# Performance work log

Measured on AMD Instinct MI355X. Metric: run time of the kernel, lower is better.

The kernel has to match this reference:

```python
import jax, jax.numpy as jnp
import numpy as np
import math


def _mixed_masks(seq_len, local_scope, num_heads, dtype=jnp.float32):
    # 4 mask groups: global (none), local band, forward (j>=i), backward (j<=i)
    i = jnp.arange(seq_len)[:, None]
    j = jnp.arange(seq_len)[None, :]
    ninf = jnp.array(-jnp.inf, dtype)
    zero = jnp.zeros((seq_len, seq_len), dtype)
    g = zero
    l = jnp.where(jnp.abs(i - j) <= local_scope, 0.0, ninf).astype(dtype)
    f = jnp.where(i > j, ninf, 0.0).astype(dtype)  # keep j >= i
    b = jnp.where(i < j, ninf, 0.0).astype(dtype)  # keep j <= i
    masks = jnp.stack([g, l, f, b], axis=0)  # [4, T, T]
    # tf.repeat(..., num_heads//4, axis=0): g,g,...,l,l,...,f,...,b,...
    return jnp.repeat(masks, num_heads // 4, axis=0)  # [H, T, T]


def setup_inputs() -> dict:
    key = jax.random.key(0)
    ks = jax.random.split(key, 6)
    B, T, D, H, dk = 2, 2048, 512, 8, 64
    return {
        "query": jax.random.normal(ks[0], (B, T, D), jnp.float32),
        "value": jax.random.normal(ks[1], (B, T, D), jnp.float32),
        "Wq": jax.random.normal(ks[2], (H, D, dk), jnp.float32) * 0.02,
        "Wk": jax.random.normal(ks[3], (H, D, dk), jnp.float32) * 0.02,
        "Wv": jax.random.normal(ks[4], (H, D, dk), jnp.float32) * 0.02,
        "Wo": jax.random.normal(ks[5], (H, dk, D), jnp.float32) * 0.02,
        "local_scope": 4,
    }


def reference(query, value, Wq, Wk, Wv, Wo, local_scope):
    B, T, D = query.shape
    H, _, dk = Wq.shape
    masks = _mixed_masks(T, local_scope, H, query.dtype)  # [H, T, T]
    # projections: 'abx,cxd->acbd'
    q = jnp.einsum('btd,hdk->bhtk', query, Wq)
    k = jnp.einsum('bsd,hdk->bhsk', value, Wk)  # key defaults to value
    v = jnp.einsum('bsd,hdk->bhsk', value, Wv)
    scores = jnp.einsum('bhtk,bhsk->bhts', q, k) / math.sqrt(dk)
    scores = scores + masks[None]  # broadcast over batch
    # Keras Softmax(axis=[-1,-2]): joint softmax over both last axes
    probs = jax.nn.softmax(scores, axis=(-2, -1))
    att = jnp.einsum('bhts,bhsk->bhtk', probs, v)
    # output projection: 'axby,xyc->abc'
    out = jnp.einsum('bhtk,hkd->btd', att, Wo)
    return out
```

## Files before the change

kernel.cpp:

```cpp
#include <hip/hip_runtime.h>
#include <math.h>

#define T_SEQ  2048
#define D_MODEL 512
#define NH     8
#define DK     64
#define NKB    32
#define BH     16
#define HK     512
#define NCH    2
#define CHB    16
#define LOG2E  1.44269504088896340736f
#define QSCALE (0.125f * LOG2E)

typedef unsigned int uint;
typedef unsigned short ushort;
typedef __attribute__((ext_vector_type(8))) short bf16x8;
typedef __attribute__((ext_vector_type(4))) float f32x4;

#define QHI_B   (0ull)
#define QLO_B   (QHI_B + 4194304ull)
#define KHI_B   (QLO_B + 4194304ull)
#define KLO_B   (KHI_B + 4194304ull)
#define VTHI_B  (KLO_B + 4194304ull)
#define VTLO_B  (VTHI_B + 4194304ull)
#define WTHI_B  (VTLO_B + 4194304ull)
#define WTLO_B  (WTHI_B + 1572864ull)
#define WOTHI_B (WTLO_B + 1572864ull)
#define WOTLO_B (WOTHI_B + 524288ull)
#define ATTP_B  (WOTLO_B + 524288ull)
#define CHUNK_F 2097152ull
#define MST_B   (ATTP_B + (ull_t)NCH * 8388608ull)
#define LST_B   (MST_B + 262144ull)
#define SST_B   (LST_B + 262144ull)
#define ATTSHI_B (SST_B + 262144ull)
#define ATTSLO_B (ATTSHI_B + 4194304ull)
typedef unsigned long long ull_t;

static __device__ __forceinline__ void tsplit2(float a, float b, uint& hi, uint& lo) {
    uint ua = __float_as_uint(a), ub = __float_as_uint(b);
    uint ha = ua & 0xFFFF0000u, hb = ub & 0xFFFF0000u;
    hi = (ha >> 16) | hb;
    float ra = a - __uint_as_float(ha);
    float rb = b - __uint_as_float(hb);
    lo = (__float_as_uint(ra) >> 16) | (__float_as_uint(rb) & 0xFFFF0000u);
}

__global__ __launch_bounds__(256) void split_w(
    const float* __restrict__ Wq, const float* __restrict__ Wk,
    const float* __restrict__ Wv, const float* __restrict__ Wo,
    float* __restrict__ ws)
{
    uint* WTH = (uint*)((char*)ws + WTHI_B);
    uint* WTL = (uint*)((char*)ws + WTLO_B);
    uint* WOH = (uint*)((char*)ws + WOTHI_B);
    uint* WOL = (uint*)((char*)ws + WOTLO_B);
    const int gid = blockIdx.x * 256 + threadIdx.x;
    if (blockIdx.x < 1536) {
        const int d2 = gid & 255;
        const int k = (gid >> 8) & 63;
        const int h = (gid >> 14) & 7;
        const int which = gid >> 17;
        const float* W = (which == 0 ? Wq : (which == 1 ? Wk : Wv));
        const float* src = W + ((size_t)h * D_MODEL + 2 * d2) * DK + k;
        uint hi, lo;
        tsplit2(src[0], src[DK], hi, lo);
        const size_t o = (((size_t)(which * 8 + h) * 64 + k) * 512 + 2 * d2) >> 1;
        WTH[o] = hi; WTL[o] = lo;
    } else {
        const int o = gid - 1536 * 256;
        const int hk2 = o & 255;
        const int d = o >> 8;
        const float* src = Wo + (size_t)(2 * hk2) * D_MODEL + d;
        uint hi, lo;
        tsplit2(src[0], src[D_MODEL], hi, lo);
        const size_t oo = ((size_t)d * 512 + 2 * hk2) >> 1;
        WOH[oo] = hi; WOL[oo] = lo;
    }
}

__global__ __launch_bounds__(256) void proj_mfma(
    const float* __restrict__ query, const float* __restrict__ value,
    float* __restrict__ ws)
{
    const int which = blockIdx.z;
    const int bh = blockIdx.y, b = bh >> 3, h = bh & 7;
    const int t0 = blockIdx.x * 64;
    const float* X = (which == 0 ? query : value) + (size_t)b * T_SEQ * D_MODEL;
    const ushort* WtH = (const ushort*)((char*)ws + WTHI_B) + (size_t)(which * 8 + h) * 64 * 512;
    const ushort* WtL = (const ushort*)((char*)ws + WTLO_B) + (size_t)(which * 8 + h) * 64 * 512;

    __shared__ ushort BsH[64][64], BsL[64][64];

    const int tid = threadIdx.x, lane = tid & 63, w = tid >> 6;
    const int lr = lane & 15, lg = lane >> 4;
    const int sg = tid & 7, srow = tid >> 3;
    const int swz0 = (sg ^ (srow & 7)) * 8;
    const int c0s = (lg ^ (lr & 7)) * 8, c1s = c0s ^ 32;

    f32x4 acc[4];
#pragma unroll
    for (int i = 0; i < 4; ++i) acc[i] = (f32x4){0.f, 0.f, 0.f, 0.f};

    for (int d0 = 0; d0 < D_MODEL; d0 += 64) {
        __syncthreads();
        *(uint4*)&BsH[srow][swz0]      = *(const uint4*)&WtH[(size_t)srow * 512 + d0 + sg * 8];
        *(uint4*)&BsH[srow + 32][swz0] = *(const uint4*)&WtH[(size_t)(srow + 32) * 512 + d0 + sg * 8];
        *(uint4*)&BsL[srow][swz0]      = *(const uint4*)&WtL[(size_t)srow * 512 + d0 + sg * 8];
        *(uint4*)&BsL[srow + 32][swz0] = *(const uint4*)&WtL[(size_t)(srow + 32) * 512 + d0 + sg * 8];
        __syncthreads();

        const float* xr = &X[(size_t)(t0 + w * 16 + lr) * D_MODEL + d0];
        float x0[8], x1[8];
        *(float4*)&x0[0] = *(const float4*)(xr + lg * 8);
        *(float4*)&x0[4] = *(const float4*)(xr + lg * 8 + 4);
        *(float4*)&x1[0] = *(const float4*)(xr + 32 + lg * 8);
        *(float4*)&x1[4] = *(const float4*)(xr + 32 + lg * 8 + 4);
        union { bf16x8 v; uint u[4]; } xh0, xl0, xh1, xl1;
#pragma unroll
        for (int i = 0; i < 4; ++i) {
            tsplit2(x0[2 * i], x0[2 * i + 1], xh0.u[i], xl0.u[i]);
            tsplit2(x1[2 * i], x1[2 * i + 1], xh1.u[i], xl1.u[i]);
        }

#pragma unroll
        for (int m2 = 0; m2 < 4; ++m2) {
            const int row = m2 * 16 + lr;
            bf16x8 wh0 = *(const bf16x8*)&BsH[row][c0s];
            bf16x8 wh1 = *(const bf16x8*)&BsH[row][c1s];
            bf16x8 wl0 = *(const bf16x8*)&BsL[row][c0s];
            bf16x8 wl1 = *(const bf16x8*)&BsL[row][c1s];
            f32x4 a = acc[m2];
            if (which < 2) {
                a = __builtin_amdgcn_mfma_f32_16x16x32_bf16(wh0, xh0.v, a, 0, 0, 0);
                a = __builtin_amdgcn_mfma_f32_16x16x32_bf16(wh1, xh1.v, a, 0, 0, 0);
                a = __builtin_amdgcn_mfma_f32_16x16x32_bf16(wh0, xl0.v, a, 0, 0, 0);
                a = __builtin_amdgcn_mfma_f32_16x16x32_bf16(wh1, xl1.v, a, 0, 0, 0);
                a = __builtin_amdgcn_mfma_f32_16x16x32_bf16(wl0, xh0.v, a, 0, 0, 0);
                a = __builtin_amdgcn_mfma_f32_16x16x32_bf16(wl1, xh1.v, a, 0, 0, 0);
            } else {
                a = __builtin_amdgcn_mfma_f32_16x16x32_bf16(xh0.v, wh0, a, 0, 0, 0);
                a = __builtin_amdgcn_mfma_f32_16x16x32_bf16(xh1.v, wh1, a, 0, 0, 0);
                a = __builtin_amdgcn_mfma_f32_16x16x32_bf16(xl0.v, wh0, a, 0, 0, 0);
                a = __builtin_amdgcn_mfma_f32_16x16x32_bf16(xl1.v, wh1, a, 0, 0, 0);
                a = __builtin_amdgcn_mfma_f32_16x16x32_bf16(xh0.v, wl0, a, 0, 0, 0);
                a = __builtin_amdgcn_mfma_f32_16x16x32_bf16(xh1.v, wl1, a, 0, 0, 0);
            }
            acc[m2] = a;
        }
    }

    if (which < 2) {
        ushort* OH = (ushort*)((char*)ws + (which == 0 ? QHI_B : KHI_B)) + (size_t)bh * T_SEQ * DK;
        ushort* OL = (ushort*)((char*)ws + (which == 0 ? QLO_B : KLO_B)) + (size_t)bh * T_SEQ * DK;
        const float scl = (which == 0) ? QSCALE : 1.0f;
#pragma unroll
        for (int m2 = 0; m2 < 4; ++m2) {
            uint h0, l0, h1, l1;
            tsplit2(acc[m2][0] * scl, acc[m2][1] * scl, h0, l0);
            tsplit2(acc[m2][2] * scl, acc[m2][3] * scl, h1, l1);
            const size_t addr = (size_t)(t0 + w * 16 + lr) * DK + m2 * 16 + lg * 4;
            *(uint2*)&OH[addr] = make_uint2(h0, h1);
            *(uint2*)&OL[addr] = make_uint2(l0, l1);
        }
    } else {
        ushort* OH = (ushort*)((char*)ws + VTHI_B) + (size_t)bh * DK * T_SEQ;
        ushort* OL = (ushort*)((char*)ws + VTLO_B) + (size_t)bh * DK * T_SEQ;
#pragma unroll
        for (int n2 = 0; n2 < 4; ++n2) {
            uint h0, l0, h1, l1;
            tsplit2(acc[n2][0], acc[n2][1], h0, l0);
            tsplit2(acc[n2][2], acc[n2][3], h1, l1);
            const size_t addr = (size_t)(n2 * 16 + lr) * T_SEQ + t0 + w * 16 + lg * 4;
            *(uint2*)&OH[addr] = make_uint2(h0, h1);
            *(uint2*)&OL[addr] = make_uint2(l0, l1);
        }
    }
}

__global__ __launch_bounds__(256, 3) void attn_fwd(
    const int* __restrict__ ls_ptr, float* __restrict__ ws)
{
    const int bh = blockIdx.y, b = bh >> 3, h = bh & 7;
    const int mtype = h >> 1;
    const int row0 = blockIdx.x * 64, rb = row0 >> 6;
    const int chunk = blockIdx.z;
    const int ls = *ls_ptr;

    float* mrow = (float*)((char*)ws + MST_B) + ((size_t)chunk * BH + bh) * T_SEQ;
    float* lrow = (float*)((char*)ws + LST_B) + ((size_t)chunk * BH + bh) * T_SEQ;

    int klo = 0, khi = NKB - 1;
    if (mtype == 1) {
        int l2 = row0 - ls; if (l2 < 0) l2 = 0;
        int h2 = row0 + 63 + ls; if (h2 > T_SEQ - 1) h2 = T_SEQ - 1;
        klo = l2 >> 6; khi = h2 >> 6;
    } else if (mtype == 2) {
        klo = rb;
    } else if (mtype == 3) {
        khi = rb;
    }
    const int kb0 = klo > chunk * CHB ? klo : chunk * CHB;
    const int kb1 = khi < chunk * CHB + CHB - 1 ? khi : chunk * CHB + CHB - 1;

    const int tid = threadIdx.x;
    if (kb0 > kb1) {
        if (tid < 64) { mrow[row0 + tid] = -INFINITY; lrow[row0 + tid] = 0.f; }
        return;
    }

    const ushort* Qh_g = (const ushort*)((char*)ws + QHI_B) + (size_t)bh * T_SEQ * DK;
    const ushort* Ql_g = (const ushort*)((char*)ws + QLO_B) + (size_t)bh * T_SEQ * DK;
    const ushort* Kh_g = (const ushort*)((char*)ws + KHI_B) + (size_t)bh * T_SEQ * DK;
    const ushort* Kl_g = (const ushort*)((char*)ws + KLO_B) + (size_t)bh * T_SEQ * DK;
    const ushort* Vh_g = (const ushort*)((char*)ws + VTHI_B) + (size_t)bh * DK * T_SEQ;
    const ushort* Vl_g = (const ushort*)((char*)ws + VTLO_B) + (size_t)bh * DK * T_SEQ;
    float* attP = (float*)((char*)ws + ATTP_B) + (size_t)chunk * CHUNK_F;

    __shared__ ushort KhS[64][64], KlS[64][64];
    __shared__ ushort VhS[64][64], VlS[64][64];
    __shared__ ushort PhS[64][64], PlS[64][64];

    const int lane = tid & 63, w = tid >> 6;
    const int lr = lane & 15, lg = lane >> 4;
    const int sg = tid & 7, srow = tid >> 3;
    const int swz0 = (sg ^ (srow & 7)) * 8;
    const int c0s = (lg ^ (lr & 7)) * 8, c1s = c0s ^ 32;

    const ushort* qh = Qh_g + (size_t)(row0 + w * 16 + lr) * DK;
    const ushort* ql = Ql_g + (size_t)(row0 + w * 16 + lr) * DK;
    const bf16x8 bqh0 = *(const bf16x8*)(qh + lg * 8);
    const bf16x8 bqh1 = *(const bf16x8*)(qh + 32 + lg * 8);
    const bf16x8 bql0 = *(const bf16x8*)(ql + lg * 8);
    const bf16x8 bql1 = *(const bf16x8*)(ql + 32 + lg * 8);

    float m_i = -INFINITY, l_i = 0.f;
    f32x4 oacc[4];
#pragma unroll
    for (int i = 0; i < 4; ++i) oacc[i] = (f32x4){0.f, 0.f, 0.f, 0.f};

    uint4 kr0, kr1, kr2, kr3, vr0, vr1, vr2, vr3;
    kr0 = *(const uint4*)&Kh_g[(size_t)(kb0 * 64 + srow) * DK + sg * 8];
    kr1 = *(const uint4*)&Kh_g[(size_t)(kb0 * 64 + srow + 32) * DK + sg * 8];
    kr2 = *(const uint4*)&Kl_g[(size_t)(kb0 * 64 + srow) * DK + sg * 8];
    kr3 = *(const uint4*)&Kl_g[(size_t)(kb0 * 64 + srow + 32) * DK + sg * 8];
    vr0 = *(const uint4*)&Vh_g[(size_t)srow * T_SEQ + kb0 * 64 + sg * 8];
    vr1 = *(const uint4*)&Vh_g[(size_t)(srow + 32) * T_SEQ + kb0 * 64 + sg * 8];
    vr2 = *(const uint4*)&Vl_g[(size_t)srow * T_SEQ + kb0 * 64 + sg * 8];
    vr3 = *(const uint4*)&Vl_g[(size_t)(srow + 32) * T_SEQ + kb0 * 64 + sg * 8];

    for (int kb = kb0; kb <= kb1; ++kb) {
        __syncthreads();
        *(uint4*)&KhS[srow][swz0] = kr0; *(uint4*)&KhS[srow + 32][swz0] = kr1;
        *(uint4*)&KlS[srow][swz0] = kr2; *(uint4*)&KlS[srow + 32][swz0] = kr3;
        *(uint4*)&VhS[srow][swz0] = vr0; *(uint4*)&VhS[srow + 32][swz0] = vr1;
        *(uint4*)&VlS[srow][swz0] = vr2; *(uint4*)&VlS[srow + 32][swz0] = vr3;
        if (kb < kb1) {
            const int kn = kb + 1;
            kr0 = *(const uint4*)&Kh_g[(size_t)(kn * 64 + srow) * DK + sg * 8];
            kr1 = *(const uint4*)&Kh_g[(size_t)(kn * 64 + srow + 32) * DK + sg * 8];
            kr2 = *(const uint4*)&Kl_g[(size_t)(kn * 64 + srow) * DK + sg * 8];
            kr3 = *(const uint4*)&Kl_g[(size_t)(kn * 64 + srow + 32) * DK + sg * 8];
            vr0 = *(const uint4*)&Vh_g[(size_t)srow * T_SEQ + kn * 64 + sg * 8];
            vr1 = *(const uint4*)&Vh_g[(size_t)(srow + 32) * T_SEQ + kn * 64 + sg * 8];
            vr2 = *(const uint4*)&Vl_g[(size_t)srow * T_SEQ + kn * 64 + sg * 8];
            vr3 = *(const uint4*)&Vl_g[(size_t)(srow + 32) * T_SEQ + kn * 64 + sg * 8];
        }
        __syncthreads();

        f32x4 sacc[4];
#pragma unroll
        for (int m = 0; m < 4; ++m) {
            const int row = m * 16 + lr;
            bf16x8 ah0 = *(const bf16x8*)&KhS[row][c0s];
            bf16x8 ah1 = *(const bf16x8*)&KhS[row][c1s];
            bf16x8 al0 = *(const bf16x8*)&KlS[row][c0s];
            bf16x8 al1 = *(const bf16x8*)&KlS[row][c1s];
            f32x4 a = (f32x4){0.f, 0.f, 0.f, 0.f};
            a = __builtin_amdgcn_mfma_f32_16x16x32_bf16(ah0, bqh0, a, 0, 0, 0);
            a = __builtin_amdgcn_mfma_f32_16x16x32_bf16(ah1, bqh1, a, 0, 0, 0);
            a = __builtin_amdgcn_mfma_f32_16x16x32_bf16(ah0, bql0, a, 0, 0, 0);
            a = __builtin_amdgcn_mfma_f32_16x16x32_bf16(ah1, bql1, a, 0, 0, 0);
            a = __builtin_amdgcn_mfma_f32_16x16x32_bf16(al0, bqh0, a, 0, 0, 0);
            a = __builtin_amdgcn_mfma_f32_16x16x32_bf16(al1, bqh1, a, 0, 0, 0);
            sacc[m] = a;
        }

        const int t_glob = row0 + w * 16 + lr;
        const bool needmask = (mtype == 1) || ((mtype >= 2) && (kb == rb));
        float p[4][4];
        float vmax = -INFINITY;
#pragma unroll
        for (int m = 0; m < 4; ++m)
#pragma unroll
            for (int r = 0; r < 4; ++r) {
                float x = sacc[m][r];
                if (needmask) {
                    int s_glob = kb * 64 + m * 16 + lg * 4 + r;
                    bool keep;
                    if (mtype == 1) keep = (t_glob - s_glob <= ls) && (s_glob - t_glob <= ls);
                    else if (mtype == 2) keep = (s_glob >= t_glob);
                    else keep = (s_glob <= t_glob);
                    if (!keep) x = -INFINITY;
                }
                p[m][r] = x;
                vmax = fmaxf(vmax, x);
            }
        vmax = fmaxf(vmax, __shfl_xor(vmax, 16, 64));
        vmax = fmaxf(vmax, __shfl_xor(vmax, 32, 64));
        const float mn = fmaxf(m_i, vmax);
        float factor = 1.f, psum = 0.f;
        if (mn == -INFINITY) {
#pragma unroll
            for (int m = 0; m < 4; ++m)
#pragma unroll
                for (int r = 0; r < 4; ++r) p[m][r] = 0.f;
        } else {
            factor = exp2f(m_i - mn);
            m_i = mn;
#pragma unroll
            for (int m = 0; m < 4; ++m)
#pragma unroll
                for (int r = 0; r < 4; ++r) {
                    p[m][r] = exp2f(p[m][r] - mn);
                    psum += p[m][r];
                }
        }
        psum += __shfl_xor(psum, 16, 64);
        psum += __shfl_xor(psum, 32, 64);
        l_i = l_i * factor + psum;

#pragma unroll
        for (int m = 0; m < 4; ++m) {
            uint ph01, pl01, ph23, pl23;
            tsplit2(p[m][0], p[m][1], ph01, pl01);
            tsplit2(p[m][2], p[m][3], ph23, pl23);
            const int pg = (((m * 2 + (lg >> 1)) ^ (lr & 7)) * 8) + (lg & 1) * 4;
            *(uint2*)&PhS[w * 16 + lr][pg] = make_uint2(ph01, ph23);
            *(uint2*)&PlS[w * 16 + lr][pg] = make_uint2(pl01, pl23);
        }

        float fr[4];
#pragma unroll
        for (int r = 0; r < 4; ++r) fr[r] = __shfl(factor, lg * 4 + r, 64);
#pragma unroll
        for (int n2 = 0; n2 < 4; ++n2)
#pragma unroll
            for (int r = 0; r < 4; ++r) oacc[n2][r] *= fr[r];

        const bf16x8 aph0 = *(const bf16x8*)&PhS[w * 16 + lr][c0s];
        const bf16x8 aph1 = *(const bf16x8*)&PhS[w * 16 + lr][c1s];
        const bf16x8 apl0 = *(const bf16x8*)&PlS[w * 16 + lr][c0s];
        const bf16x8 apl1 = *(const bf16x8*)&PlS[w * 16 + lr][c1s];
#pragma unroll
        for (int n2 = 0; n2 < 4; ++n2) {
            const int row = n2 * 16 + lr;
            bf16x8 bh0 = *(const bf16x8*)&VhS[row][c0s];
            bf16x8 bh1 = *(const bf16x8*)&VhS[row][c1s];
            bf16x8 bl0 = *(const bf16x8*)&VlS[row][c0s];
            bf16x8 bl1 = *(const bf16x8*)&VlS[row][c1s];
            f32x4 a = oacc[n2];
            a = __builtin_amdgcn_mfma_f32_16x16x32_bf16(aph0, bh0, a, 0, 0, 0);
            a = __builtin_amdgcn_mfma_f32_16x16x32_bf16(aph1, bh1, a, 0, 0, 0);
            a = __builtin_amdgcn_mfma_f32_16x16x32_bf16(aph0, bl0, a, 0, 0, 0);
            a = __builtin_amdgcn_mfma_f32_16x16x32_bf16(aph1, bl1, a, 0, 0, 0);
            a = __builtin_amdgcn_mfma_f32_16x16x32_bf16(apl0, bh0, a, 0, 0, 0);
            a = __builtin_amdgcn_mfma_f32_16x16x32_bf16(apl1, bh1, a, 0, 0, 0);
            oacc[n2] = a;
        }
    }

#pragma unroll
    for (int n2 = 0; n2 < 4; ++n2)
#pragma unroll
        for (int r = 0; r < 4; ++r) {
            int t = row0 + w * 16 + lg * 4 + r;
            attP[((size_t)b * T_SEQ + t) * HK + h * DK + n2 * 16 + lr] = oacc[n2][r];
        }
    if (lg == 0) {
        mrow[row0 + w * 16 + lr] = m_i;
        lrow[row0 + w * 16 + lr] = l_i;
    }
}

__global__ __launch_bounds__(256) void softmax_stats(float* __restrict__ ws)
{
    const int bh = blockIdx.x;
    float* mbase = (float*)((char*)ws + MST_B);
    float* lbase = (float*)((char*)ws + LST_B);
    float* sbase = (float*)((char*)ws + SST_B);

    __shared__ float red[256];
    const int tid = threadIdx.x;
    const int n = NCH * T_SEQ;

    float mymax = -INFINITY;
    for (int i = tid; i < n; i += 256) {
        int c = i >> 11, t = i & 2047;
        mymax = fmaxf(mymax, mbase[((size_t)c * BH + bh) * T_SEQ + t]);
    }
    red[tid] = mymax; __syncthreads();
    for (int s = 128; s > 0; s >>= 1) {
        if (tid < s) red[tid] = fmaxf(red[tid], red[tid + s]);
        __syncthreads();
    }
    const float M = red[0]; __syncthreads();

    float mysum = 0.f;
    for (int i = tid; i < n; i += 256) {
        int c = i >> 11, t = i & 2047;
        size_t idx = ((size_t)c * BH + bh) * T_SEQ + t;
        mysum += lbase[idx] * exp2f(mbase[idx] - M);
    }
    red[tid] = mysum; __syncthreads();
    for (int s = 128; s > 0; s >>= 1) {
        if (tid < s) red[tid] += red[tid + s];
        __syncthreads();
    }
    const float Z = red[0];

    for (int i = tid; i < n; i += 256) {
        int c = i >> 11, t = i & 2047;
        size_t idx = ((size_t)c * BH + bh) * T_SEQ + t;
        sbase[idx] = exp2f(mbase[idx] - M) / Z;
    }
}

__global__ __launch_bounds__(256) void reduce_split(float* __restrict__ ws)
{
    const size_t flat = ((size_t)blockIdx.x * 256 + threadIdx.x) * 4;
    const float* attP = (const float*)((char*)ws + ATTP_B);
    const float* sc = (const float*)((char*)ws + SST_B);
    ushort* SH = (ushort*)((char*)ws + ATTSHI_B);
    ushort* SL = (ushort*)((char*)ws + ATTSLO_B);

    const int hk = (int)(flat & (HK - 1));
    const size_t bt = flat / HK;
    const int b = (int)(bt >> 11), t = (int)(bt & 2047);
    const int h = hk >> 6;

    float4 acc = make_float4(0.f, 0.f, 0.f, 0.f);
    for (int c = 0; c < NCH; ++c) {
        float4 a = *(const float4*)&attP[(size_t)c * CHUNK_F + flat];
        float s = sc[((size_t)c * BH + b * NH + h) * T_SEQ + t];
        acc.x = fmaf(a.x, s, acc.x); acc.y = fmaf(a.y, s, acc.y);
        acc.z = fmaf(a.z, s, acc.z); acc.w = fmaf(a.w, s, acc.w);
    }
    uint h0, l0, h1, l1;
    tsplit2(acc.x, acc.y, h0, l0);
    tsplit2(acc.z, acc.w, h1, l1);
    *(uint2*)&SH[flat] = make_uint2(h0, h1);
    *(uint2*)&SL[flat] = make_uint2(l0, l1);
}

__global__ __launch_bounds__(256) void out_proj_mfma(
    float* __restrict__ ws, float* __restrict__ out)
{
    const int d0 = blockIdx.x * 64;
    const int r0 = blockIdx.y * 64;
    const ushort* AH = (const ushort*)((char*)ws + ATTSHI_B);
    const ushort* AL = (const ushort*)((char*)ws + ATTSLO_B);
    const ushort* WoH = (const ushort*)((char*)ws + WOTHI_B);
    const ushort* WoL = (const ushort*)((char*)ws + WOTLO_B);

    __shared__ ushort BsH[64][64], BsL[64][64];

    const int tid = threadIdx.x, lane = tid & 63, w = tid >> 6;
    const int lr = lane & 15, lg = lane >> 4;
    const int sg = tid & 7, srow = tid >> 3;
    const int swz0 = (sg ^ (srow & 7)) * 8;
    const int c0s = (lg ^ (lr & 7)) * 8, c1s = c0s ^ 32;

    f32x4 acc[4];
#pragma unroll
    for (int i = 0; i < 4; ++i) acc[i] = (f32x4){0.f, 0.f, 0.f, 0.f};

    for (int k0 = 0; k0 < HK; k0 += 64) {
        __syncthreads();
        *(uint4*)&BsH[srow][swz0]      = *(const uint4*)&WoH[(size_t)(d0 + srow) * HK + k0 + sg * 8];
        *(uint4*)&BsH[srow + 32][swz0] = *(const uint4*)&WoH[(size_t)(d0 + srow + 32) * HK + k0 + sg * 8];
        *(uint4*)&BsL[srow][swz0]      = *(const uint4*)&WoL[(size_t)(d0 + srow) * HK + k0 + sg * 8];
        *(uint4*)&BsL[srow + 32][swz0] = *(const uint4*)&WoL[(size_t)(d0 + srow + 32) * HK + k0 + sg * 8];
        __syncthreads();

        const ushort* ar = AH + (size_t)(r0 + w * 16 + lr) * HK + k0;
        const ushort* al = AL + (size_t)(r0 + w * 16 + lr) * HK + k0;
        bf16x8 ah0 = *(const bf16x8*)(ar + lg * 8);
        bf16x8 ah1 = *(const bf16x8*)(ar + 32 + lg * 8);
        bf16x8 al0 = *(const bf16x8*)(al + lg * 8);
        bf16x8 al1 = *(const bf16x8*)(al + 32 + lg * 8);

#pragma unroll
        for (int n2 = 0; n2 < 4; ++n2) {
            const int row = n2 * 16 + lr;
            bf16x8 wh0 = *(const bf16x8*)&BsH[row][c0s];
            bf16x8 wh1 = *(const bf16x8*)&BsH[row][c1s];
            bf16x8 wl0 = *(const bf16x8*)&BsL[row][c0s];
            bf16x8 wl1 = *(const bf16x8*)&BsL[row][c1s];
            f32x4 a = acc[n2];
            a = __builtin_amdgcn_mfma_f32_16x16x32_bf16(ah0, wh0, a, 0, 0, 0);
            a = __builtin_amdgcn_mfma_f32_16x16x32_bf16(ah1, wh1, a, 0, 0, 0);
            a = __builtin_amdgcn_mfma_f32_16x16x32_bf16(ah0, wl0, a, 0, 0, 0);
            a = __builtin_amdgcn_mfma_f32_16x16x32_bf16(ah1, wl1, a, 0, 0, 0);
            a = __builtin_amdgcn_mfma_f32_16x16x32_bf16(al0, wh0, a, 0, 0, 0);
            a = __builtin_amdgcn_mfma_f32_16x16x32_bf16(al1, wh1, a, 0, 0, 0);
            acc[n2] = a;
        }
    }

#pragma unroll
    for (int n2 = 0; n2 < 4; ++n2)
#pragma unroll
        for (int i = 0; i < 4; ++i)
            out[(size_t)(r0 + w * 16 + lg * 4 + i) * D_MODEL + d0 + n2 * 16 + lr] = acc[n2][i];
}

extern "C" void kernel_launch(void* const* d_in, const int* in_sizes, int n_in,
                              void* d_out, int out_size, void* d_ws, size_t ws_size,
                              hipStream_t stream)
{
    const float* query = (const float*)d_in[0];
    const float* value = (const float*)d_in[1];
    const float* Wq = (const float*)d_in[2];
    const float* Wk = (const float*)d_in[3];
    const float* Wv = (const float*)d_in[4];
    const float* Wo = (const float*)d_in[5];
    const int* ls = (const int*)d_in[6];
    float* out = (float*)d_out;
    float* ws = (float*)d_ws;

    split_w<<<dim3(2048), 256, 0, stream>>>(Wq, Wk, Wv, Wo, ws);

    proj_mfma<<<dim3(T_SEQ / 64, BH, 3), 256, 0, stream>>>(query, value, ws);

    attn_fwd<<<dim3(T_SEQ / 64, BH, NCH), 256, 0, stream>>>(ls, ws);

    softmax_stats<<<dim3(BH), 256, 0, stream>>>(ws);

    reduce_split<<<dim3(2 * T_SEQ * HK / 1024), 256, 0, stream>>>(ws);

    out_proj_mfma<<<dim3(D_MODEL / 64, 2 * T_SEQ / 64), 256, 0, stream>>>(ws, out);
}
```

Measured before the change: 140.6 us.

## Fuse QKV projections into one kernel and fold split-reduce into output projection

The three Q/K/V projection launches are merged into one kernel that loads the weight tiles for all three into shared memory and reuses the value-input split for both the K and V projections. The separate reduce_split pass, which combined the two attention chunks with softmax scales and wrote hi/lo bf16 buffers, is folded into the output projection. That kernel now reads the fp32 partials directly, scales, splits and multiplies against Wo read from global memory without shared-memory staging. The attn_fwd launch bound is also lowered from 3 to 2 waves-per-EU. This removes a launch and an intermediate buffer round-trip, at the cost of more registers and shared memory in the fused projection and uncached global Wo reads.

Result: slower. 161.6 us (+15.0%).

```diff
diff --git a/kernel.cpp b/kernel.cpp
--- a/kernel.cpp
+++ b/kernel.cpp
@@ -15,6 +15,7 @@
 
 typedef unsigned int uint;
 typedef unsigned short ushort;
+typedef unsigned long long ull_t;
 typedef __attribute__((ext_vector_type(8))) short bf16x8;
 typedef __attribute__((ext_vector_type(4))) float f32x4;
 
@@ -33,9 +34,6 @@
 #define MST_B   (ATTP_B + (ull_t)NCH * 8388608ull)
 #define LST_B   (MST_B + 262144ull)
 #define SST_B   (LST_B + 262144ull)
-#define ATTSHI_B (SST_B + 262144ull)
-#define ATTSLO_B (ATTSHI_B + 4194304ull)
-typedef unsigned long long ull_t;
 
 static __device__ __forceinline__ void tsplit2(float a, float b, uint& hi, uint& lo) {
     uint ua = __float_as_uint(a), ub = __float_as_uint(b);
@@ -79,18 +77,18 @@
     }
 }
 
-__global__ __launch_bounds__(256) void proj_mfma(
+__global__ __launch_bounds__(256) void proj_fused(
     const float* __restrict__ query, const float* __restrict__ value,
     float* __restrict__ ws)
 {
-    const int which = blockIdx.z;
     const int bh = blockIdx.y, b = bh >> 3, h = bh & 7;
     const int t0 = blockIdx.x * 64;
-    const float* X = (which == 0 ? query : value) + (size_t)b * T_SEQ * D_MODEL;
-    const ushort* WtH = (const ushort*)((char*)ws + WTHI_B) + (size_t)(which * 8 + h) * 64 * 512;
-    const ushort* WtL = (const ushort*)((char*)ws + WTLO_B) + (size_t)(which * 8 + h) * 64 * 512;
-
-    __shared__ ushort BsH[64][64], BsL[64][64];
+    const float* Xq = query + (size_t)b * T_SEQ * D_MODEL;
+    const float* Xv = value + (size_t)b * T_SEQ * D_MODEL;
+    const ushort* WH = (const ushort*)((char*)ws + WTHI_B);
+    const ushort* WL = (const ushort*)((char*)ws + WTLO_B);
+
+    __shared__ ushort BsH[3][64][64], BsL[3][64][64];
 
     const int tid = threadIdx.x, lane = tid & 63, w = tid >> 6;
     const int lr = lane & 15, lg = lane >> 4;
@@ -98,79 +96,137 @@
     const int swz0 = (sg ^ (srow & 7)) * 8;
     const int c0s = (lg ^ (lr & 7)) * 8, c1s = c0s ^ 32;
 
-    f32x4 acc[4];
-#pragma unroll
-    for (int i = 0; i < 4; ++i) acc[i] = (f32x4){0.f, 0.f, 0.f, 0.f};
+    f32x4 accq[4], acck[4], accv[4];
+#pragma unroll
+    for (int i = 0; i < 4; ++i) {
+        accq[i] = (f32x4){0.f, 0.f, 0.f, 0.f};
+        acck[i] = (f32x4){0.f, 0.f, 0.f, 0.f};
+        accv[i] = (f32x4){0.f, 0.f, 0.f, 0.f};
+    }
 
     for (int d0 = 0; d0 < D_MODEL; d0 += 64) {
         __syncthreads();
-        *(uint4*)&BsH[srow][swz0]      = *(const uint4*)&WtH[(size_t)srow * 512 + d0 + sg * 8];
-        *(uint4*)&BsH[srow + 32][swz0] = *(const uint4*)&WtH[(size_t)(srow + 32) * 512 + d0 + sg * 8];
-        *(uint4*)&BsL[srow][swz0]      = *(const uint4*)&WtL[(size_t)srow * 512 + d0 + sg * 8];
-        *(uint4*)&BsL[srow + 32][swz0] = *(const uint4*)&WtL[(size_t)(srow + 32) * 512 + d0 + sg * 8];
+#pragma unroll
+        for (int wq = 0; wq < 3; ++wq) {
+            const ushort* sH = WH + (size_t)(wq * 8 + h) * 64 * 512;
+            const ushort* sL = WL + (size_t)(wq * 8 + h) * 64 * 512;
+            *(uint4*)&BsH[wq][srow][swz0]      = *(const uint4*)&sH[(size_t)srow * 512 + d0 + sg * 8];
+            *(uint4*)&BsH[wq][srow + 32][swz0] = *(const uint4*)&sH[(size_t)(srow + 32) * 512 + d0 + sg * 8];
+            *(uint4*)&BsL[wq][srow][swz0]      = *(const uint4*)&sL[(size_t)srow * 512 + d0 + sg * 8];
+            *(uint4*)&BsL[wq][srow + 32][swz0] = *(const uint4*)&sL[(size_t)(srow + 32) * 512 + d0 + sg * 8];
+        }
         __syncthreads();
 
-        const float* xr = &X[(size_t)(t0 + w * 16 + lr) * D_MODEL + d0];
-        float x0[8], x1[8];
-        *(float4*)&x0[0] = *(const float4*)(xr + lg * 8);
-        *(float4*)&x0[4] = *(const float4*)(xr + lg * 8 + 4);
-        *(float4*)&x1[0] = *(const float4*)(xr + 32 + lg * 8);
-        *(float4*)&x1[4] = *(const float4*)(xr + 32 + lg * 8 + 4);
-        union { bf16x8 v; uint u[4]; } xh0, xl0, xh1, xl1;
-#pragma unroll
-        for (int i = 0; i < 4; ++i) {
-            tsplit2(x0[2 * i], x0[2 * i + 1], xh0.u[i], xl0.u[i]);
-            tsplit2(x1[2 * i], x1[2 * i + 1], xh1.u[i], xl1.u[i]);
+        union { bf16x8 v; uint u[4]; } qh0, ql0, qh1, ql1, vh0, vl0, vh1, vl1;
+        {
+            const float* xr = &Xq[(size_t)(t0 + w * 16 + lr) * D_MODEL + d0];
+            float x0[8], x1[8];
+            *(float4*)&x0[0] = *(const float4*)(xr + lg * 8);
+            *(float4*)&x0[4] = *(const float4*)(xr + lg * 8 + 4);
+            *(float4*)&x1[0] = *(const float4*)(xr + 32 + lg * 8);
+            *(float4*)&x1[4] = *(const float4*)(xr + 32 + lg * 8 + 4);
+#pragma unroll
+            for (int i = 0; i < 4; ++i) {
+                tsplit2(x0[2 * i], x0[2 * i + 1], qh0.u[i], ql0.u[i]);
+                tsplit2(x1[2 * i], x1[2 * i + 1], qh1.u[i], ql1.u[i]);
+            }
+        }
+        {
+            const float* xr = &Xv[(size_t)(t0 + w * 16 + lr) * D_MODEL + d0];
+            float x0[8], x1[8];
+            *(float4*)&x0[0] = *(const float4*)(xr + lg * 8);
+            *(float4*)&x0[4] = *(const float4*)(xr + lg * 8 + 4);
+            *(float4*)&x1[0] = *(const float4*)(xr + 32 + lg * 8);
+            *(float4*)&x1[4] = *(const float4*)(xr + 32 + lg * 8 + 4);
+#pragma unroll
+            for (int i = 0; i < 4; ++i) {
+                tsplit2(x0[2 * i], x0[2 * i + 1], vh0.u[i], vl0.u[i]);
+                tsplit2(x1[2 * i], x1[2 * i + 1], vh1.u[i], vl1.u[i]);
+            }
         }
 
 #pragma unroll
         for (int m2 = 0; m2 < 4; ++m2) {
             const int row = m2 * 16 + lr;
-            bf16x8 wh0 = *(const bf16x8*)&BsH[row][c0s];
-            bf16x8 wh1 = *(const bf16x8*)&BsH[row][c1s];
-            bf16x8 wl0 = *(const bf16x8*)&BsL[row][c0s];
-            bf16x8 wl1 = *(const bf16x8*)&BsL[row][c1s];
-            f32x4 a = acc[m2];
-            if (which < 2) {
-                a = __builtin_amdgcn_mfma_f32_16x16x32_bf16(wh0, xh0.v, a, 0, 0, 0);
-                a = __builtin_amdgcn_mfma_f32_16x16x32_bf16(wh1, xh1.v, a, 0, 0, 0);
-                a = __builtin_amdgcn_mfma_f32_16x16x32_bf16(wh0, xl0.v, a, 0, 0, 0);
-                a = __builtin_amdgcn_mfma_f32_16x16x32_bf16(wh1, xl1.v, a, 0, 0, 0);
-                a = __builtin_amdgcn_mfma_f32_16x16x32_bf16(wl0, xh0.v, a, 0, 0, 0);
-                a = __builtin_amdgcn_mfma_f32_16x16x32_bf16(wl1, xh1.v, a, 0, 0, 0);
-            } else {
-                a = __builtin_amdgcn_mfma_f32_16x16x32_bf16(xh0.v, wh0, a, 0, 0, 0);
-                a = __builtin_amdgcn_mfma_f32_16x16x32_bf16(xh1.v, wh1, a, 0, 0, 0);
-                a = __builtin_amdgcn_mfma_f32_16x16x32_bf16(xl0.v, wh0, a, 0, 0, 0);
-                a = __builtin_amdgcn_mfma_f32_16x16x32_bf16(xl1.v, wh1, a, 0, 0, 0);
-                a = __builtin_amdgcn_mfma_f32_16x16x32_bf16(xh0.v, wl0, a, 0, 0, 0);
-                a = __builtin_amdgcn_mfma_f32_16x16x32_bf16(xh1.v, wl1, a, 0, 0, 0);
-            }
-            acc[m2] = a;
-        }
-    }
-
-    if (which < 2) {
-        ushort* OH = (ushort*)((char*)ws + (which == 0 ? QHI_B : KHI_B)) + (size_t)bh * T_SEQ * DK;
-        ushort* OL = (ushort*)((char*)ws + (which == 0 ? QLO_B : KLO_B)) + (size_t)bh * T_SEQ * DK;
-        const float scl = (which == 0) ? QSCALE : 1.0f;
+            {
+                bf16x8 wh0 = *(const bf16x8*)&BsH[0][row][c0s];
+                bf16x8 wh1 = *(const bf16x8*)&BsH[0][row][c1s];
+                bf16x8 wl0 = *(const bf16x8*)&BsL[0][row][c0s];
+                bf16x8 wl1 = *(const bf16x8*)&BsL[0][row][c1s];
+                f32x4 a = accq[m2];
+                a = __builtin_amdgcn_mfma_f32_16x16x32_bf16(wh0, qh0.v, a, 0, 0, 0);
+                a = __builtin_amdgcn_mfma_f32_16x16x32_bf16(wh1, qh1.v, a, 0, 0, 0);
+                a = __builtin_amdgcn_mfma_f32_16x16x32_bf16(wh0, ql0.v, a, 0, 0, 0);
+                a = __builtin_amdgcn_mfma_f32_16x16x32_bf16(wh1, ql1.v, a, 0, 0, 0);
+                a = __builtin_amdgcn_mfma_f32_16x16x32_bf16(wl0, qh0.v, a, 0, 0, 0);
+                a = __builtin_amdgcn_mfma_f32_16x16x32_bf16(wl1, qh1.v, a, 0, 0, 0);
+                accq[m2] = a;
+            }
+            {
+                bf16x8 wh0 = *(const bf16x8*)&BsH[1][row][c0s];
+                bf16x8 wh1 = *(const bf16x8*)&BsH[1][row][c1s];
+                bf16x8 wl0 = *(const bf16x8*)&BsL[1][row][c0s];
+                bf16x8 wl1 = *(const bf16x8*)&BsL[1][row][c1s];
+                f32x4 a = acck[m2];
+                a = __builtin_amdgcn_mfma_f32_16x16x32_bf16(wh0, vh0.v, a, 0, 0, 0);
+                a = __builtin_amdgcn_mfma_f32_16x16x32_bf16(wh1, vh1.v, a, 0, 0, 0);
+                a = __builtin_amdgcn_mfma_f32_16x16x32_bf16(wh0, vl0.v, a, 0, 0, 0);
+                a = __builtin_amdgcn_mfma_f32_16x16x32_bf16(wh1, vl1.v, a, 0, 0, 0);
+                a = __builtin_amdgcn_mfma_f32_16x16x32_bf16(wl0, vh0.v, a, 0, 0, 0);
+                a = __builtin_amdgcn_mfma_f32_16x16x32_bf16(wl1, vh1.v, a, 0, 0, 0);
+                acck[m2] = a;
+            }
+            {
+                bf16x8 wh0 = *(const bf16x8*)&BsH[2][row][c0s];
+                bf16x8 wh1 = *(const bf16x8*)&BsH[2][row][c1s];
+                bf16x8 wl0 = *(const bf16x8*)&BsL[2][row][c0s];
+                bf16x8 wl1 = *(const bf16x8*)&BsL[2][row][c1s];
+                f32x4 a = accv[m2];
+                a = __builtin_amdgcn_mfma_f32_16x16x32_bf16(vh0.v, wh0, a, 0, 0, 0);
+                a = __builtin_amdgcn_mfma_f32_16x16x32_bf16(vh1.v, wh1, a, 0, 0, 0);
+                a = __builtin_amdgcn_mfma_f32_16x16x32_bf16(vl0.v, wh0, a, 0, 0, 0);
+                a = __builtin_amdgcn_mfma_f32_16x16x32_bf16(vl1.v, wh1, a, 0, 0, 0);
+                a = __builtin_amdgcn_mfma_f32_16x16x32_bf16(vh0.v, wl0, a, 0, 0, 0);
+                a = __builtin_amdgcn_mfma_f32_16x16x32_bf16(vh1.v, wl1, a, 0, 0, 0);
+                accv[m2] = a;
+            }
+        }
+    }
+
+    {
+        ushort* OH = (ushort*)((char*)ws + QHI_B) + (size_t)bh * T_SEQ * DK;
+        ushort* OL = (ushort*)((char*)ws + QLO_B) + (size_t)bh * T_SEQ * DK;
 #pragma unroll
         for (int m2 = 0; m2 < 4; ++m2) {
             uint h0, l0, h1, l1;
-            tsplit2(acc[m2][0] * scl, acc[m2][1] * scl, h0, l0);
-            tsplit2(acc[m2][2] * scl, acc[m2][3] * scl, h1, l1);
+            tsplit2(accq[m2][0] * QSCALE, accq[m2][1] * QSCALE, h0, l0);
+            tsplit2(accq[m2][2] * QSCALE, accq[m2][3] * QSCALE, h1, l1);
             const size_t addr = (size_t)(t0 + w * 16 + lr) * DK + m2 * 16 + lg * 4;
             *(uint2*)&OH[addr] = make_uint2(h0, h1);
             *(uint2*)&OL[addr] = make_uint2(l0, l1);
         }
-    } else {
+    }
+    {
+        ushort* OH = (ushort*)((char*)ws + KHI_B) + (size_t)bh * T_SEQ * DK;
+        ushort* OL = (ushort*)((char*)ws + KLO_B) + (size_t)bh * T_SEQ * DK;
+#pragma unroll
+        for (int m2 = 0; m2 < 4; ++m2) {
+            uint h0, l0, h1, l1;
+            tsplit2(acck[m2][0], acck[m2][1], h0, l0);
+            tsplit2(acck[m2][2], acck[m2][3], h1, l1);
+            const size_t addr = (size_t)(t0 + w * 16 + lr) * DK + m2 * 16 + lg * 4;
+            *(uint2*)&OH[addr] = make_uint2(h0, h1);
+            *(uint2*)&OL[addr] = make_uint2(l0, l1);
+        }
+    }
+    {
         ushort* OH = (ushort*)((char*)ws + VTHI_B) + (size_t)bh * DK * T_SEQ;
         ushort* OL = (ushort*)((char*)ws + VTLO_B) + (size_t)bh * DK * T_SEQ;
 #pragma unroll
         for (int n2 = 0; n2 < 4; ++n2) {
             uint h0, l0, h1, l1;
-            tsplit2(acc[n2][0], acc[n2][1], h0, l0);
-            tsplit2(acc[n2][2], acc[n2][3], h1, l1);
+            tsplit2(accv[n2][0], accv[n2][1], h0, l0);
+            tsplit2(accv[n2][2], accv[n2][3], h1, l1);
             const size_t addr = (size_t)(n2 * 16 + lr) * T_SEQ + t0 + w * 16 + lg * 4;
             *(uint2*)&OH[addr] = make_uint2(h0, h1);
             *(uint2*)&OL[addr] = make_uint2(l0, l1);
@@ -178,7 +234,7 @@
     }
 }
 
-__global__ __launch_bounds__(256, 3) void attn_fwd(
+__global__ __launch_bounds__(256, 2) void attn_fwd(
     const int* __restrict__ ls_ptr, float* __restrict__ ws)
 {
     const int bh = blockIdx.y, b = bh >> 3, h = bh & 7;
@@ -426,93 +482,71 @@
     }
 }
 
-__global__ __launch_bounds__(256) void reduce_split(float* __restrict__ ws)
+__global__ __launch_bounds__(256) void out_fused(
+    float* __restrict__ ws, float* __restrict__ out)
 {
-    const size_t flat = ((size_t)blockIdx.x * 256 + threadIdx.x) * 4;
+    const int d0 = blockIdx.x * 128;
+    const int grow0 = blockIdx.y * 64;
+    const int b = grow0 >> 11;
+    const int t0 = grow0 & 2047;
     const float* attP = (const float*)((char*)ws + ATTP_B);
     const float* sc = (const float*)((char*)ws + SST_B);
-    ushort* SH = (ushort*)((char*)ws + ATTSHI_B);
-    ushort* SL = (ushort*)((char*)ws + ATTSLO_B);
-
-    const int hk = (int)(flat & (HK - 1));
-    const size_t bt = flat / HK;
-    const int b = (int)(bt >> 11), t = (int)(bt & 2047);
-    const int h = hk >> 6;
-
-    float4 acc = make_float4(0.f, 0.f, 0.f, 0.f);
-    for (int c = 0; c < NCH; ++c) {
-        float4 a = *(const float4*)&attP[(size_t)c * CHUNK_F + flat];
-        float s = sc[((size_t)c * BH + b * NH + h) * T_SEQ + t];
-        acc.x = fmaf(a.x, s, acc.x); acc.y = fmaf(a.y, s, acc.y);
-        acc.z = fmaf(a.z, s, acc.z); acc.w = fmaf(a.w, s, acc.w);
-    }
-    uint h0, l0, h1, l1;
-    tsplit2(acc.x, acc.y, h0, l0);
-    tsplit2(acc.z, acc.w, h1, l1);
-    *(uint2*)&SH[flat] = make_uint2(h0, h1);
-    *(uint2*)&SL[flat] = make_uint2(l0, l1);
-}
-
-__global__ __launch_bounds__(256) void out_proj_mfma(
-    float* __restrict__ ws, float* __restrict__ out)
-{
-    const int d0 = blockIdx.x * 64;
-    const int r0 = blockIdx.y * 64;
-    const ushort* AH = (const ushort*)((char*)ws + ATTSHI_B);
-    const ushort* AL = (const ushort*)((char*)ws + ATTSLO_B);
-    const ushort* WoH = (const ushort*)((char*)ws + WOTHI_B);
-    const ushort* WoL = (const ushort*)((char*)ws + WOTLO_B);
-
-    __shared__ ushort BsH[64][64], BsL[64][64];
+    const ushort* WOH = (const ushort*)((char*)ws + WOTHI_B);
+    const ushort* WOL = (const ushort*)((char*)ws + WOTLO_B);
 
     const int tid = threadIdx.x, lane = tid & 63, w = tid >> 6;
     const int lr = lane & 15, lg = lane >> 4;
-    const int sg = tid & 7, srow = tid >> 3;
-    const int swz0 = (sg ^ (srow & 7)) * 8;
-    const int c0s = (lg ^ (lr & 7)) * 8, c1s = c0s ^ 32;
-
-    f32x4 acc[4];
-#pragma unroll
-    for (int i = 0; i < 4; ++i) acc[i] = (f32x4){0.f, 0.f, 0.f, 0.f};
+    const int t_lane = t0 + w * 16 + lr;
+    const float* aP = attP + ((size_t)b * T_SEQ + t_lane) * HK;
+
+    f32x4 acc[8];
+#pragma unroll
+    for (int i = 0; i < 8; ++i) acc[i] = (f32x4){0.f, 0.f, 0.f, 0.f};
 
     for (int k0 = 0; k0 < HK; k0 += 64) {
-        __syncthreads();
-        *(uint4*)&BsH[srow][swz0]      = *(const uint4*)&WoH[(size_t)(d0 + srow) * HK + k0 + sg * 8];
-        *(uint4*)&BsH[srow + 32][swz0] = *(const uint4*)&WoH[(size_t)(d0 + srow + 32) * HK + k0 + sg * 8];
-        *(uint4*)&BsL[srow][swz0]      = *(const uint4*)&WoL[(size_t)(d0 + srow) * HK + k0 + sg * 8];
-        *(uint4*)&BsL[srow + 32][swz0] = *(const uint4*)&WoL[(size_t)(d0 + srow + 32) * HK + k0 + sg * 8];
-        __syncthreads();
-
-        const ushort* ar = AH + (size_t)(r0 + w * 16 + lr) * HK + k0;
-        const ushort* al = AL + (size_t)(r0 + w * 16 + lr) * HK + k0;
-        bf16x8 ah0 = *(const bf16x8*)(ar + lg * 8);
-        bf16x8 ah1 = *(const bf16x8*)(ar + 32 + lg * 8);
-        bf16x8 al0 = *(const bf16x8*)(al + lg * 8);
-        bf16x8 al1 = *(const bf16x8*)(al + 32 + lg * 8);
-
-#pragma unroll
-        for (int n2 = 0; n2 < 4; ++n2) {
-            const int row = n2 * 16 + lr;
-            bf16x8 wh0 = *(const bf16x8*)&BsH[row][c0s];
-            bf16x8 wh1 = *(const bf16x8*)&BsH[row][c1s];
-            bf16x8 wl0 = *(const bf16x8*)&BsL[row][c0s];
-            bf16x8 wl1 = *(const bf16x8*)&BsL[row][c1s];
-            f32x4 a = acc[n2];
-            a = __builtin_amdgcn_mfma_f32_16x16x32_bf16(ah0, wh0, a, 0, 0, 0);
-            a = __builtin_amdgcn_mfma_f32_16x16x32_bf16(ah1, wh1, a, 0, 0, 0);
-            a = __builtin_amdgcn_mfma_f32_16x16x32_bf16(ah0, wl0, a, 0, 0, 0);
-            a = __builtin_amdgcn_mfma_f32_16x16x32_bf16(ah1, wl1, a, 0, 0, 0);
-            a = __builtin_amdgcn_mfma_f32_16x16x32_bf16(al0, wh0, a, 0, 0, 0);
-            a = __builtin_amdgcn_mfma_f32_16x16x32_bf16(al1, wh1, a, 0, 0, 0);
-            acc[n2] = a;
-        }
-    }
-
-#pragma unroll
-    for (int n2 = 0; n2 < 4; ++n2)
+        const int h = k0 >> 6;
+        const float s0 = sc[((size_t)0 * BH + b * NH + h) * T_SEQ + t_lane];
+        const float s1 = sc[((size_t)1 * BH + b * NH + h) * T_SEQ + t_lane];
+
+        union { bf16x8 v; uint u[4]; } ah[2], al[2];
+#pragma unroll
+        for (int kh = 0; kh < 2; ++kh) {
+            const float* p = aP + k0 + kh * 32 + lg * 8;
+            float4 x0 = *(const float4*)(p);
+            float4 x1 = *(const float4*)(p + 4);
+            float4 y0 = *(const float4*)(p + CHUNK_F);
+            float4 y1 = *(const float4*)(p + CHUNK_F + 4);
+            float v[8];
+            v[0] = x0.x * s0 + y0.x * s1; v[1] = x0.y * s0 + y0.y * s1;
+            v[2] = x0.z * s0 + y0.z * s1; v[3] = x0.w * s0 + y0.w * s1;
+            v[4] = x1.x * s0 + y1.x * s1; v[5] = x1.y * s0 + y1.y * s1;
+            v[6] = x1.z * s0 + y1.z * s1; v[7] = x1.w * s0 + y1.w * s1;
+#pragma unroll
+            for (int i = 0; i < 4; ++i)
+                tsplit2(v[2 * i], v[2 * i + 1], ah[kh].u[i], al[kh].u[i]);
+        }
+
+#pragma unroll
+        for (int dg = 0; dg < 8; ++dg) {
+            const size_t dbase = (size_t)(d0 + dg * 16 + lr) * HK + k0;
+#pragma unroll
+            for (int kh = 0; kh < 2; ++kh) {
+                bf16x8 bhf = *(const bf16x8*)&WOH[dbase + kh * 32 + lg * 8];
+                bf16x8 blf = *(const bf16x8*)&WOL[dbase + kh * 32 + lg * 8];
+                f32x4 a = acc[dg];
+                a = __builtin_amdgcn_mfma_f32_16x16x32_bf16(ah[kh].v, bhf, a, 0, 0, 0);
+                a = __builtin_amdgcn_mfma_f32_16x16x32_bf16(ah[kh].v, blf, a, 0, 0, 0);
+                a = __builtin_amdgcn_mfma_f32_16x16x32_bf16(al[kh].v, bhf, a, 0, 0, 0);
+                acc[dg] = a;
+            }
+        }
+    }
+
+#pragma unroll
+    for (int dg = 0; dg < 8; ++dg)
 #pragma unroll
         for (int i = 0; i < 4; ++i)
-            out[(size_t)(r0 + w * 16 + lg * 4 + i) * D_MODEL + d0 + n2 * 16 + lr] = acc[n2][i];
+            out[(size_t)(grow0 + w * 16 + lg * 4 + i) * D_MODEL + d0 + dg * 16 + lr] = acc[dg][i];
 }
 
 extern "C" void kernel_launch(void* const* d_in, const int* in_sizes, int n_in,
@@ -531,13 +565,11 @@
 
     split_w<<<dim3(2048), 256, 0, stream>>>(Wq, Wk, Wv, Wo, ws);
 
-    proj_mfma<<<dim3(T_SEQ / 64, BH, 3), 256, 0, stream>>>(query, value, ws);
+    proj_fused<<<dim3(T_SEQ / 64, BH), 256, 0, stream>>>(query, value, ws);
 
     attn_fwd<<<dim3(T_SEQ / 64, BH, NCH), 256, 0, stream>>>(ls, ws);
 
     softmax_stats<<<dim3(BH), 256, 0, stream>>>(ws);
 
-    reduce_split<<<dim3(2 * T_SEQ * HK / 1024), 256, 0, stream>>>(ws);
-
-    out_proj_mfma<<<dim3(D_MODEL / 64, 2 * T_SEQ / 64), 256, 0, stream>>>(ws, out);
-}
+    out_fused<<<dim3(D_MODEL / 128, 2 * T_SEQ / 64), 256, 0, stream>>>(ws, out);
+}
```

## Load K/V fragments directly from global memory, drop LDS staging and syncs

Applied to the files above, without the earlier changes.

The attention kernel no longer stages K and V tiles through shared memory with register prefetch and two barriers per key block. Each wave now reads its MFMA operand fragments straight from global memory, relying on L1/L2 for reuse across the four waves. This frees LDS so occupancy can rise to 4 blocks, and the grid is flattened to 1D with bh as the fastest index so that blocks sharing K/V run close together. The cost is four-fold redundant global/cache traffic per block and no explicit prefetch to hide load latency.

Result: slower. 313.8 us (+123.2%).

```diff
diff --git a/kernel.cpp b/kernel.cpp
--- a/kernel.cpp
+++ b/kernel.cpp
@@ -15,6 +15,7 @@
 
 typedef unsigned int uint;
 typedef unsigned short ushort;
+typedef unsigned long long ull_t;
 typedef __attribute__((ext_vector_type(8))) short bf16x8;
 typedef __attribute__((ext_vector_type(4))) float f32x4;
 
@@ -35,7 +36,6 @@
 #define SST_B   (LST_B + 262144ull)
 #define ATTSHI_B (SST_B + 262144ull)
 #define ATTSLO_B (ATTSHI_B + 4194304ull)
-typedef unsigned long long ull_t;
 
 static __device__ __forceinline__ void tsplit2(float a, float b, uint& hi, uint& lo) {
     uint ua = __float_as_uint(a), ub = __float_as_uint(b);
@@ -178,13 +178,15 @@
     }
 }
 
-__global__ __launch_bounds__(256, 3) void attn_fwd(
+__global__ __launch_bounds__(256, 4) void attn_fwd(
     const int* __restrict__ ls_ptr, float* __restrict__ ws)
 {
-    const int bh = blockIdx.y, b = bh >> 3, h = bh & 7;
+    const int id = blockIdx.x;
+    const int bh = id & 15, b = bh >> 3, h = bh & 7;
+    const int r2 = id >> 4;
+    const int tile = r2 & 31, chunk = r2 >> 5;
     const int mtype = h >> 1;
-    const int row0 = blockIdx.x * 64, rb = row0 >> 6;
-    const int chunk = blockIdx.z;
+    const int row0 = tile * 64, rb = tile;
     const int ls = *ls_ptr;
 
     float* mrow = (float*)((char*)ws + MST_B) + ((size_t)chunk * BH + bh) * T_SEQ;
@@ -217,14 +219,10 @@
     const ushort* Vl_g = (const ushort*)((char*)ws + VTLO_B) + (size_t)bh * DK * T_SEQ;
     float* attP = (float*)((char*)ws + ATTP_B) + (size_t)chunk * CHUNK_F;
 
-    __shared__ ushort KhS[64][64], KlS[64][64];
-    __shared__ ushort VhS[64][64], VlS[64][64];
     __shared__ ushort PhS[64][64], PlS[64][64];
 
     const int lane = tid & 63, w = tid >> 6;
     const int lr = lane & 15, lg = lane >> 4;
-    const int sg = tid & 7, srow = tid >> 3;
-    const int swz0 = (sg ^ (srow & 7)) * 8;
     const int c0s = (lg ^ (lr & 7)) * 8, c1s = c0s ^ 32;
 
     const ushort* qh = Qh_g + (size_t)(row0 + w * 16 + lr) * DK;
@@ -239,43 +237,16 @@
 #pragma unroll
     for (int i = 0; i < 4; ++i) oacc[i] = (f32x4){0.f, 0.f, 0.f, 0.f};
 
-    uint4 kr0, kr1, kr2, kr3, vr0, vr1, vr2, vr3;
-    kr0 = *(const uint4*)&Kh_g[(size_t)(kb0 * 64 + srow) * DK + sg * 8];
-    kr1 = *(const uint4*)&Kh_g[(size_t)(kb0 * 64 + srow + 32) * DK + sg * 8];
-    kr2 = *(const uint4*)&Kl_g[(size_t)(kb0 * 64 + srow) * DK + sg * 8];
-    kr3 = *(const uint4*)&Kl_g[(size_t)(kb0 * 64 + srow + 32) * DK + sg * 8];
-    vr0 = *(const uint4*)&Vh_g[(size_t)srow * T_SEQ + kb0 * 64 + sg * 8];
-    vr1 = *(const uint4*)&Vh_g[(size_t)(srow + 32) * T_SEQ + kb0 * 64 + sg * 8];
-    vr2 = *(const uint4*)&Vl_g[(size_t)srow * T_SEQ + kb0 * 64 + sg * 8];
-    vr3 = *(const uint4*)&Vl_g[(size_t)(srow + 32) * T_SEQ + kb0 * 64 + sg * 8];
-
     for (int kb = kb0; kb <= kb1; ++kb) {
-        __syncthreads();
-        *(uint4*)&KhS[srow][swz0] = kr0; *(uint4*)&KhS[srow + 32][swz0] = kr1;
-        *(uint4*)&KlS[srow][swz0] = kr2; *(uint4*)&KlS[srow + 32][swz0] = kr3;
-        *(uint4*)&VhS[srow][swz0] = vr0; *(uint4*)&VhS[srow + 32][swz0] = vr1;
-        *(uint4*)&VlS[srow][swz0] = vr2; *(uint4*)&VlS[srow + 32][swz0] = vr3;
-        if (kb < kb1) {
-            const int kn = kb + 1;
-            kr0 = *(const uint4*)&Kh_g[(size_t)(kn * 64 + srow) * DK + sg * 8];
-            kr1 = *(const uint4*)&Kh_g[(size_t)(kn * 64 + srow + 32) * DK + sg * 8];
-            kr2 = *(const uint4*)&Kl_g[(size_t)(kn * 64 + srow) * DK + sg * 8];
-            kr3 = *(const uint4*)&Kl_g[(size_t)(kn * 64 + srow + 32) * DK + sg * 8];
-            vr0 = *(const uint4*)&Vh_g[(size_t)srow * T_SEQ + kn * 64 + sg * 8];
-            vr1 = *(const uint4*)&Vh_g[(size_t)(srow + 32) * T_SEQ + kn * 64 + sg * 8];
-            vr2 = *(const uint4*)&Vl_g[(size_t)srow * T_SEQ + kn * 64 + sg * 8];
-            vr3 = *(const uint4*)&Vl_g[(size_t)(srow + 32) * T_SEQ + kn * 64 + sg * 8];
-        }
-        __syncthreads();
-
         f32x4 sacc[4];
 #pragma unroll
         for (int m = 0; m < 4; ++m) {
-            const int row = m * 16 + lr;
-            bf16x8 ah0 = *(const bf16x8*)&KhS[row][c0s];
-            bf16x8 ah1 = *(const bf16x8*)&KhS[row][c1s];
-            bf16x8 al0 = *(const bf16x8*)&KlS[row][c0s];
-            bf16x8 al1 = *(const bf16x8*)&KlS[row][c1s];
+            const ushort* krh = Kh_g + (size_t)(kb * 64 + m * 16 + lr) * DK;
+            const ushort* krl = Kl_g + (size_t)(kb * 64 + m * 16 + lr) * DK;
+            bf16x8 ah0 = *(const bf16x8*)(krh + lg * 8);
+            bf16x8 ah1 = *(const bf16x8*)(krh + 32 + lg * 8);
+            bf16x8 al0 = *(const bf16x8*)(krl + lg * 8);
+            bf16x8 al1 = *(const bf16x8*)(krl + 32 + lg * 8);
             f32x4 a = (f32x4){0.f, 0.f, 0.f, 0.f};
             a = __builtin_amdgcn_mfma_f32_16x16x32_bf16(ah0, bqh0, a, 0, 0, 0);
             a = __builtin_amdgcn_mfma_f32_16x16x32_bf16(ah1, bqh1, a, 0, 0, 0);
@@ -354,11 +325,12 @@
         const bf16x8 apl1 = *(const bf16x8*)&PlS[w * 16 + lr][c1s];
 #pragma unroll
         for (int n2 = 0; n2 < 4; ++n2) {
-            const int row = n2 * 16 + lr;
-            bf16x8 bh0 = *(const bf16x8*)&VhS[row][c0s];
-            bf16x8 bh1 = *(const bf16x8*)&VhS[row][c1s];
-            bf16x8 bl0 = *(const bf16x8*)&VlS[row][c0s];
-            bf16x8 bl1 = *(const bf16x8*)&VlS[row][c1s];
+            const ushort* vrh = Vh_g + (size_t)(n2 * 16 + lr) * T_SEQ + kb * 64;
+            const ushort* vrl = Vl_g + (size_t)(n2 * 16 + lr) * T_SEQ + kb * 64;
+            bf16x8 bh0 = *(const bf16x8*)(vrh + lg * 8);
+            bf16x8 bh1 = *(const bf16x8*)(vrh + 32 + lg * 8);
+            bf16x8 bl0 = *(const bf16x8*)(vrl + lg * 8);
+            bf16x8 bl1 = *(const bf16x8*)(vrl + 32 + lg * 8);
             f32x4 a = oacc[n2];
             a = __builtin_amdgcn_mfma_f32_16x16x32_bf16(aph0, bh0, a, 0, 0, 0);
             a = __builtin_amdgcn_mfma_f32_16x16x32_bf16(aph1, bh1, a, 0, 0, 0);
@@ -533,7 +505,7 @@
 
     proj_mfma<<<dim3(T_SEQ / 64, BH, 3), 256, 0, stream>>>(query, value, ws);
 
-    attn_fwd<<<dim3(T_SEQ / 64, BH, NCH), 256, 0, stream>>>(ls, ws);
+    attn_fwd<<<dim3((T_SEQ / 64) * BH * NCH), 256, 0, stream>>>(ls, ws);
 
     softmax_stats<<<dim3(BH), 256, 0, stream>>>(ws);
 
```
